# Kernel optimization log

Measured on AMD Instinct MI355X. Metric: run time of the kernel, lower is better.

Reference implementation:

```python
import jax, jax.numpy as jnp
import numpy as np

N_NODES = 100000
N_EDGE_PAIRS = 800000  # undirected pairs -> 1.6M directed edges
DIM_IN = 128
NUM_CLASSES = 16
N_ITERS = 5


def _log_normalize(a):
    return a - jax.nn.logsumexp(a, axis=-1, keepdims=True)


def setup_inputs() -> dict:
    key = jax.random.key(0)
    k1, k2, k3, k4, k5 = jax.random.split(key, 5)
    # reciprocal directed edges: edges 2i and 2i+1 are reverses of each other
    src = jax.random.randint(k1, (N_EDGE_PAIRS,), 0, N_NODES)
    dst = jax.random.randint(k2, (N_EDGE_PAIRS,), 0, N_NODES)
    e_src = jnp.stack([src, dst], axis=1).reshape(-1)  # [E]
    e_dst = jnp.stack([dst, src], axis=1).reshape(-1)  # [E]
    edge_index = jnp.stack([e_src, e_dst], axis=0)     # [2, E]
    E = e_src.shape[0]
    rv = jnp.arange(E).reshape(-1, 2)[:, ::-1].reshape(-1)  # reverse-edge permutation
    x = jax.random.normal(k3, (N_NODES, DIM_IN), dtype=jnp.float32)
    W = jax.random.normal(k4, (DIM_IN, NUM_CLASSES), dtype=jnp.float32) * 0.1
    b = jnp.zeros((NUM_CLASSES,), dtype=jnp.float32)
    dim_param = NUM_CLASSES * (NUM_CLASSES + 1) // 2
    param = jax.random.normal(k5, (dim_param,), dtype=jnp.float32) * 0.1
    return {"x": x, "W": W, "b": b, "param": param,
            "edge_index": edge_index, "rv": rv}


def reference(x, W, b, param, edge_index, rv):
    N = x.shape[0]
    C = W.shape[1]
    # MLP (num_hidden=0 -> single Linear) + LogSoftmax
    log_b0 = jax.nn.log_softmax(x @ W + b, axis=-1)  # [N, C]
    # coupling matrix logH (symmetric), detached since learn_coupling=False
    rid, cid = np.tril_indices(C)
    logT = jnp.zeros((C, C), dtype=x.dtype).at[rid, cid].set(
        jax.nn.log_sigmoid(param * 10.0))
    logH = logT + jnp.triu(logT.T, 1)
    logH = jax.lax.stop_gradient(logH)
    src, dst = edge_index[0], edge_index[1]
    E = src.shape[0]
    log_msg = jnp.full((E, C), -float(np.log(C)), dtype=x.dtype)
    log_b = log_b0
    for _ in range(N_ITERS):
        # message: gather beliefs at source, subtract reverse message
        t = log_b[src] - log_msg[rv]                                    # [E, C]
        raw = jax.nn.logsumexp(t[:, :, None] + logH[None, :, :], axis=1)  # [E, C]
        log_msg = _log_normalize(raw)
        # aggregate (scatter-add) into destination nodes, then update
        agg = jax.ops.segment_sum(log_msg, dst, num_segments=N)         # [N, C]
        log_b = _log_normalize(agg + log_b0)
    return log_b
```

## Files before the change

### kernel.cpp

```cpp
#include <hip/hip_runtime.h>
#include <math.h>

#define NN      100000
#define EE      1600000
#define NPAIRS  800000
#define DIN     128
#define CC      16
#define NITERS  5
#define PPT     4
#define NGRP    (NPAIRS / PPT)

__device__ __forceinline__ unsigned short f2bf(float f) {
    unsigned int u = __float_as_uint(f);
    unsigned int r = u + 0x7fffu + ((u >> 16) & 1u);
    return (unsigned short)(r >> 16);
}
__device__ __forceinline__ unsigned int pack_bf(float lo, float hi) {
    return (unsigned int)f2bf(lo) | ((unsigned int)f2bf(hi) << 16);
}

__global__ __launch_bounds__(256) void k_logb0(
    const float* __restrict__ x, const float* __restrict__ W,
    const float* __restrict__ b, float* __restrict__ logb0)
{
    int idx  = blockIdx.x * blockDim.x + threadIdx.x;
    int node = idx >> 4;
    int c    = idx & 15;
    if (node >= NN) return;
    const float* xr = x + (long)node * DIN;
    float acc = b[c];
#pragma unroll 8
    for (int k = 0; k < DIN; ++k)
        acc = fmaf(xr[k], W[k * CC + c], acc);
    float m = acc;
    for (int off = 8; off; off >>= 1) m = fmaxf(m, __shfl_xor(m, off, 16));
    float s = __expf(acc - m);
    for (int off = 8; off; off >>= 1) s += __shfl_xor(s, off, 16);
    logb0[idx] = acc - m - __logf(s);
}

__global__ void k_M(const float* __restrict__ param, float* __restrict__ M)
{
    int i = threadIdx.x;
    if (i >= CC * (CC + 1) / 2) return;
    int r = 0;
    while ((r + 1) * (r + 2) / 2 <= i) ++r;
    int c = i - r * (r + 1) / 2;
    float z = param[i] * 10.0f;
    float s = 1.0f / (1.0f + __expf(-z));
    M[r * CC + c] = s;
    if (r != c) M[c * CC + r] = s;
}

__global__ void k_init(unsigned int* __restrict__ msg2, float* __restrict__ agg)
{
    const float NEGLOGC = -2.772588722239781f;
    unsigned int v = pack_bf(NEGLOGC, NEGLOGC);
    long stride = (long)gridDim.x * blockDim.x;
    long i0 = (long)blockIdx.x * blockDim.x + threadIdx.x;
    for (long j = i0; j < (long)NPAIRS * CC; j += stride) msg2[j] = v;
    for (long j = i0; j < (long)NN * CC; j += stride) agg[j] = 0.f;
}

__global__ __launch_bounds__(256) void k_edges(
    const int* __restrict__ esrc, const int* __restrict__ edst,
    const float* __restrict__ logb, const float* __restrict__ Mg,
    unsigned int* __restrict__ msg2, float* __restrict__ agg)
{
    __shared__ float sM[CC * CC];
    __shared__ float sE[16 * 40];
    sM[threadIdx.x] = Mg[threadIdx.x];
    __syncthreads();

    const int lane = threadIdx.x & 15;
    const int gl   = threadIdx.x >> 4;
    const int g    = blockIdx.x * 16 + gl;
    float* eb = sE + gl * 40;

    float Hrow[CC];
#pragma unroll
    for (int k = 0; k < CC; ++k) Hrow[k] = sM[k * CC + lane];

#pragma unroll
    for (int r = 0; r < PPT; ++r) {
        const long p  = (long)g + (long)r * NGRP;
        const long e0 = 2 * p;

        int2 s01 = *(const int2*)(esrc + e0);
        int2 d01 = *(const int2*)(edst + e0);

        unsigned int mold = msg2[p * CC + lane];
        float mo0 = __uint_as_float(mold << 16);
        float mo1 = __uint_as_float(mold & 0xffff0000u);

        float t0 = logb[(long)s01.x * CC + lane] - mo1;
        float t1 = logb[(long)s01.y * CC + lane] - mo0;

        eb[lane]      = __expf(t0);
        eb[16 + lane] = __expf(t1);
        float ev0[CC], ev1[CC];
        *(float4*)(ev0 +  0) = *(const float4*)(eb +  0);
        *(float4*)(ev0 +  4) = *(const float4*)(eb +  4);
        *(float4*)(ev0 +  8) = *(const float4*)(eb +  8);
        *(float4*)(ev0 + 12) = *(const float4*)(eb + 12);
        *(float4*)(ev1 +  0) = *(const float4*)(eb + 16);
        *(float4*)(ev1 +  4) = *(const float4*)(eb + 20);
        *(float4*)(ev1 +  8) = *(const float4*)(eb + 24);
        *(float4*)(ev1 + 12) = *(const float4*)(eb + 28);

        float S0 = 0.f, S1 = 0.f;
#pragma unroll
        for (int k = 0; k < CC; ++k) {
            S0 = fmaf(ev0[k], Hrow[k], S0);
            S1 = fmaf(ev1[k], Hrow[k], S1);
        }

        float T0 = S0, T1 = S1;
        for (int off = 8; off; off >>= 1) {
            T0 += __shfl_xor(T0, off, 16);
            T1 += __shfl_xor(T1, off, 16);
        }
        float n0 = __logf(S0) - __logf(T0);
        float n1 = __logf(S1) - __logf(T1);

        msg2[p * CC + lane] = pack_bf(n0, n1);

        atomicAdd(&agg[(long)d01.x * CC + lane], n0);
        atomicAdd(&agg[(long)d01.y * CC + lane], n1);
    }
}

__global__ __launch_bounds__(256) void k_update(
    const float* __restrict__ logb0, float* __restrict__ agg,
    float* __restrict__ out)
{
    int idx  = blockIdx.x * blockDim.x + threadIdx.x;
    int node = idx >> 4;
    if (node >= NN) return;
    float v = agg[idx] + logb0[idx];
    agg[idx] = 0.f;
    float m = v;
    for (int off = 8; off; off >>= 1) m = fmaxf(m, __shfl_xor(m, off, 16));
    float s = __expf(v - m);
    for (int off = 8; off; off >>= 1) s += __shfl_xor(s, off, 16);
    out[idx] = v - m - __logf(s);
}

extern "C" void kernel_launch(void* const* d_in, const int* in_sizes, int n_in,
                              void* d_out, int out_size, void* d_ws, size_t ws_size,
                              hipStream_t stream)
{
    const float* x     = (const float*)d_in[0];
    const float* W     = (const float*)d_in[1];
    const float* b     = (const float*)d_in[2];
    const float* param = (const float*)d_in[3];
    const int*   eidx  = (const int*)d_in[4];
    const int*   esrc  = eidx;
    const int*   edst  = eidx + EE;

    float* ws    = (float*)d_ws;
    float* M     = ws;
    float* logb0 = M     + 256;
    float* logb  = logb0 + (long)NN * CC;
    float* agg   = logb  + (long)NN * CC;
    unsigned int* msg2 = (unsigned int*)(agg + (long)NN * CC);

    k_logb0<<<(NN * CC + 255) / 256, 256, 0, stream>>>(x, W, b, logb0);
    k_M    <<<1, 256, 0, stream>>>(param, M);
    k_init <<<2048, 256, 0, stream>>>(msg2, agg);

    const float* curb = logb0;
    for (int it = 0; it < NITERS; ++it) {
        k_edges<<<NGRP * 16 / 256, 256, 0, stream>>>(esrc, edst, curb, M, msg2, agg);
        float* dst = (it == NITERS - 1) ? (float*)d_out : logb;
        k_update<<<(NN * CC + 255) / 256, 256, 0, stream>>>(logb0, agg, dst);
        curb = dst;
    }
}
```

Before: 615.9 us.

## Specialize edge kernel per iteration, drop message init, batch loads, fuse setup

Templates the edge kernel so the first iteration uses the constant initial message instead of reading it, and the last iteration skips writing messages. This removes the full message-init pass and one read and one write of the message buffer. All index and message loads for the four pairs are issued up front with nontemporal hints to overlap gather latency. The setup kernels are merged into one launch with vectorized x loads. Shared memory grows to per-pair staging buffers, and bounds checks are dropped on the assumption that sizes divide evenly.

```diff
diff --git a/kernel.cpp b/kernel.cpp
--- a/kernel.cpp
+++ b/kernel.cpp
@@ -9,6 +9,10 @@
 #define NITERS  5
 #define PPT     4
 #define NGRP    (NPAIRS / PPT)
+#define NEGLOGC (-2.772588722239781f)
+
+typedef float  f4 __attribute__((ext_vector_type(4)));
+typedef int    i2 __attribute__((ext_vector_type(2)));
 
 __device__ __forceinline__ unsigned short f2bf(float f) {
     unsigned int u = __float_as_uint(f);
@@ -19,19 +23,37 @@
     return (unsigned int)f2bf(lo) | ((unsigned int)f2bf(hi) << 16);
 }
 
-__global__ __launch_bounds__(256) void k_logb0(
+__global__ __launch_bounds__(256) void k_setup(
     const float* __restrict__ x, const float* __restrict__ W,
-    const float* __restrict__ b, float* __restrict__ logb0)
+    const float* __restrict__ b, const float* __restrict__ param,
+    float* __restrict__ M, float* __restrict__ logb0, float* __restrict__ agg)
 {
-    int idx  = blockIdx.x * blockDim.x + threadIdx.x;
+    if (blockIdx.x == 0 && threadIdx.x < CC * (CC + 1) / 2) {
+        int i = threadIdx.x;
+        int r = 0;
+        while ((r + 1) * (r + 2) / 2 <= i) ++r;
+        int c = i - r * (r + 1) / 2;
+        float z = param[i] * 10.0f;
+        float s = 1.0f / (1.0f + __expf(-z));
+        M[r * CC + c] = s;
+        if (r != c) M[c * CC + r] = s;
+    }
+
+    int idx  = blockIdx.x * 256 + threadIdx.x;
+    agg[idx] = 0.f;
+
     int node = idx >> 4;
-    int c    = idx & 15;
-    if (node >= NN) return;
-    const float* xr = x + (long)node * DIN;
-    float acc = b[c];
+    int cls  = idx & 15;
+    const f4* xr4 = (const f4*)(x + (long)node * DIN);
+    float acc = b[cls];
 #pragma unroll 8
-    for (int k = 0; k < DIN; ++k)
-        acc = fmaf(xr[k], W[k * CC + c], acc);
+    for (int k4 = 0; k4 < DIN / 4; ++k4) {
+        f4 xv = __builtin_nontemporal_load(xr4 + k4);
+        acc = fmaf(xv.x, W[(4 * k4 + 0) * CC + cls], acc);
+        acc = fmaf(xv.y, W[(4 * k4 + 1) * CC + cls], acc);
+        acc = fmaf(xv.z, W[(4 * k4 + 2) * CC + cls], acc);
+        acc = fmaf(xv.w, W[(4 * k4 + 3) * CC + cls], acc);
+    }
     float m = acc;
     for (int off = 8; off; off >>= 1) m = fmaxf(m, __shfl_xor(m, off, 16));
     float s = __expf(acc - m);
@@ -39,65 +61,55 @@
     logb0[idx] = acc - m - __logf(s);
 }
 
-__global__ void k_M(const float* __restrict__ param, float* __restrict__ M)
-{
-    int i = threadIdx.x;
-    if (i >= CC * (CC + 1) / 2) return;
-    int r = 0;
-    while ((r + 1) * (r + 2) / 2 <= i) ++r;
-    int c = i - r * (r + 1) / 2;
-    float z = param[i] * 10.0f;
-    float s = 1.0f / (1.0f + __expf(-z));
-    M[r * CC + c] = s;
-    if (r != c) M[c * CC + r] = s;
-}
-
-__global__ void k_init(unsigned int* __restrict__ msg2, float* __restrict__ agg)
-{
-    const float NEGLOGC = -2.772588722239781f;
-    unsigned int v = pack_bf(NEGLOGC, NEGLOGC);
-    long stride = (long)gridDim.x * blockDim.x;
-    long i0 = (long)blockIdx.x * blockDim.x + threadIdx.x;
-    for (long j = i0; j < (long)NPAIRS * CC; j += stride) msg2[j] = v;
-    for (long j = i0; j < (long)NN * CC; j += stride) agg[j] = 0.f;
-}
-
-__global__ __launch_bounds__(256) void k_edges(
-    const int* __restrict__ esrc, const int* __restrict__ edst,
+template <bool RD_MSG, bool WR_MSG>
+__global__ __launch_bounds__(256) void k_edges_t(
+    const i2* __restrict__ esrc2, const i2* __restrict__ edst2,
     const float* __restrict__ logb, const float* __restrict__ Mg,
     unsigned int* __restrict__ msg2, float* __restrict__ agg)
 {
     __shared__ float sM[CC * CC];
-    __shared__ float sE[16 * 40];
+    __shared__ float sE[PPT][16 * 40];
     sM[threadIdx.x] = Mg[threadIdx.x];
     __syncthreads();
 
     const int lane = threadIdx.x & 15;
     const int gl   = threadIdx.x >> 4;
     const int g    = blockIdx.x * 16 + gl;
-    float* eb = sE + gl * 40;
 
     float Hrow[CC];
 #pragma unroll
     for (int k = 0; k < CC; ++k) Hrow[k] = sM[k * CC + lane];
 
+    i2 s01[PPT], d01[PPT];
+    unsigned int mold[PPT];
 #pragma unroll
     for (int r = 0; r < PPT; ++r) {
-        const long p  = (long)g + (long)r * NGRP;
-        const long e0 = 2 * p;
+        int p = g + r * NGRP;
+        s01[r] = __builtin_nontemporal_load(esrc2 + p);
+        d01[r] = __builtin_nontemporal_load(edst2 + p);
+        if (RD_MSG)
+            mold[r] = __builtin_nontemporal_load(msg2 + (long)p * CC + lane);
+    }
 
-        int2 s01 = *(const int2*)(esrc + e0);
-        int2 d01 = *(const int2*)(edst + e0);
+#pragma unroll
+    for (int r = 0; r < PPT; ++r) {
+        float lb0 = logb[(long)s01[r].x * CC + lane];
+        float lb1 = logb[(long)s01[r].y * CC + lane];
+        float mo0, mo1;
+        if (RD_MSG) {
+            mo0 = __uint_as_float(mold[r] << 16);
+            mo1 = __uint_as_float(mold[r] & 0xffff0000u);
+        } else {
+            mo0 = NEGLOGC; mo1 = NEGLOGC;
+        }
+        float* eb = sE[r] + gl * 40;
+        eb[lane]      = __expf(lb0 - mo1);
+        eb[16 + lane] = __expf(lb1 - mo0);
+    }
 
-        unsigned int mold = msg2[p * CC + lane];
-        float mo0 = __uint_as_float(mold << 16);
-        float mo1 = __uint_as_float(mold & 0xffff0000u);
-
-        float t0 = logb[(long)s01.x * CC + lane] - mo1;
-        float t1 = logb[(long)s01.y * CC + lane] - mo0;
-
-        eb[lane]      = __expf(t0);
-        eb[16 + lane] = __expf(t1);
+#pragma unroll
+    for (int r = 0; r < PPT; ++r) {
+        const float* eb = sE[r] + gl * 40;
         float ev0[CC], ev1[CC];
         *(float4*)(ev0 +  0) = *(const float4*)(eb +  0);
         *(float4*)(ev0 +  4) = *(const float4*)(eb +  4);
@@ -123,10 +135,13 @@
         float n0 = __logf(S0) - __logf(T0);
         float n1 = __logf(S1) - __logf(T1);
 
-        msg2[p * CC + lane] = pack_bf(n0, n1);
-
-        atomicAdd(&agg[(long)d01.x * CC + lane], n0);
-        atomicAdd(&agg[(long)d01.y * CC + lane], n1);
+        if (WR_MSG) {
+            int p = g + r * NGRP;
+            __builtin_nontemporal_store(pack_bf(n0, n1),
+                                        msg2 + (long)p * CC + lane);
+        }
+        atomicAdd(&agg[(long)d01[r].x * CC + lane], n0);
+        atomicAdd(&agg[(long)d01[r].y * CC + lane], n1);
     }
 }
 
@@ -134,9 +149,7 @@
     const float* __restrict__ logb0, float* __restrict__ agg,
     float* __restrict__ out)
 {
-    int idx  = blockIdx.x * blockDim.x + threadIdx.x;
-    int node = idx >> 4;
-    if (node >= NN) return;
+    int idx = blockIdx.x * blockDim.x + threadIdx.x;
     float v = agg[idx] + logb0[idx];
     agg[idx] = 0.f;
     float m = v;
@@ -155,8 +168,8 @@
     const float* b     = (const float*)d_in[2];
     const float* param = (const float*)d_in[3];
     const int*   eidx  = (const int*)d_in[4];
-    const int*   esrc  = eidx;
-    const int*   edst  = eidx + EE;
+    const i2*    esrc2 = (const i2*)eidx;
+    const i2*    edst2 = (const i2*)(eidx + EE);
 
     float* ws    = (float*)d_ws;
     float* M     = ws;
@@ -165,15 +178,21 @@
     float* agg   = logb  + (long)NN * CC;
     unsigned int* msg2 = (unsigned int*)(agg + (long)NN * CC);
 
-    k_logb0<<<(NN * CC + 255) / 256, 256, 0, stream>>>(x, W, b, logb0);
-    k_M    <<<1, 256, 0, stream>>>(param, M);
-    k_init <<<2048, 256, 0, stream>>>(msg2, agg);
+    k_setup<<<NN * CC / 256, 256, 0, stream>>>(x, W, b, param, M, logb0, agg);
 
     const float* curb = logb0;
     for (int it = 0; it < NITERS; ++it) {
-        k_edges<<<NGRP * 16 / 256, 256, 0, stream>>>(esrc, edst, curb, M, msg2, agg);
+        if (it == 0)
+            k_edges_t<false, true><<<NGRP / 16, 256, 0, stream>>>(
+                esrc2, edst2, curb, M, msg2, agg);
+        else if (it == NITERS - 1)
+            k_edges_t<true, false><<<NGRP / 16, 256, 0, stream>>>(
+                esrc2, edst2, curb, M, msg2, agg);
+        else
+            k_edges_t<true, true><<<NGRP / 16, 256, 0, stream>>>(
+                esrc2, edst2, curb, M, msg2, agg);
         float* dst = (it == NITERS - 1) ? (float*)d_out : logb;
-        k_update<<<(NN * CC + 255) / 256, 256, 0, stream>>>(logb0, agg, dst);
+        k_update<<<NN * CC / 256, 256, 0, stream>>>(logb0, agg, dst);
         curb = dst;
     }
 }
```

Measured after the change: 612.8 us. About the same (-0.5%).
